# Kernel tuning notes

Hardware: AMD Instinct MI355X
Metric: run time of the kernel (lower is better)

## Reference

```python
import jax, jax.numpy as jnp
import numpy as np

B, S, O = 65536, 32, 16  # batch, state_dim, observation_dim


def setup_inputs() -> dict:
    key = jax.random.key(0)
    k1, k2, k3, k4 = jax.random.split(key, 4)
    observation = jax.random.normal(k1, (B, O), dtype=jnp.float32)
    # SPD observation noise covariance per batch element
    L = 0.1 * jax.random.normal(k2, (B, O, O), dtype=jnp.float32)
    observation_noise = jnp.einsum('bij,bkj->bik', L, L) + 1e-3 * jnp.eye(O, dtype=jnp.float32)
    observation_matrix = 0.001 * jax.random.normal(k3, (O, S), dtype=jnp.float32)
    observation_bias = 1e-6 * jax.random.normal(k4, (O,), dtype=jnp.float32)
    prior_mean = jnp.zeros((S,), dtype=jnp.float32)
    prior_precision = jnp.eye(S, dtype=jnp.float32)
    return {
        'observation': observation,
        'observation_noise': observation_noise,
        'observation_matrix': observation_matrix,
        'observation_bias': observation_bias,
        'prior_mean': prior_mean,
        'prior_precision': prior_precision,
    }


def reference(observation, observation_noise, observation_matrix, observation_bias,
              prior_mean, prior_precision):
    # observation: [B, O]; observation_noise: [B, O, O]
    noise_prec = jnp.linalg.inv(observation_noise)                      # [B, O, O]
    HtR = jnp.einsum('os,bop->bsp', observation_matrix, noise_prec)     # H^T R^{-1}: [B, S, O]
    innovation_cov = jnp.einsum('bso,ot->bst', HtR, observation_matrix) # [B, S, S]
    posterior_covariance = jnp.linalg.inv(prior_precision + innovation_cov)  # [B, S, S]
    residual = jnp.einsum('bso,bo->bs', HtR, observation - observation_bias)[..., None]  # [B, S, 1]
    prior_term = (prior_precision @ prior_mean)[:, None]                # [S, 1]
    posterior_mean = posterior_covariance @ (prior_term + residual)     # [B, S, 1]
    return posterior_mean, posterior_covariance
```

## Files before the change

kernel.cpp:

```cpp
#include <hip/hip_runtime.h>
#include <hip/hip_bf16.h>


typedef __attribute__((ext_vector_type(8))) short bf16x8;
typedef __attribute__((ext_vector_type(4))) float f32x4;

__device__ __forceinline__ unsigned bf16rne(float f) {
    unsigned x = __float_as_uint(f);
    return (x + 0x7FFFu + ((x >> 16) & 1u)) >> 16;
}
__device__ __forceinline__ unsigned pack2(float a, float b) {
    return bf16rne(a) | (bf16rne(b) << 16);
}

__global__ void lgs_setup(const float* __restrict__ H, const float* __restrict__ bias,
                          const float* __restrict__ mu0, const float* __restrict__ P,
                          float* __restrict__ ws)
{
    __shared__ float aug[32][65];
    __shared__ float colk[32];
    __shared__ float Gs[16][32];
    __shared__ float Gts[32][16];
    const int tid = threadIdx.x;

    for (int idx = tid; idx < 2048; idx += 256) {
        int r = idx >> 6, c = idx & 63;
        aug[r][c] = (c < 32) ? P[r * 32 + c] : (((c - 32) == r) ? 1.0f : 0.0f);
    }
    __syncthreads();

    for (int k = 0; k < 32; ++k) {
        if (tid < 32) colk[tid] = aug[tid][k];
        __syncthreads();
        if (tid < 64) {
            float rk = aug[k][tid] * (1.0f / colk[k]);
            aug[k][tid] = rk;
            for (int r = 0; r < 32; ++r)
                if (r != k) aug[r][tid] -= colk[r] * rk;
        }
        __syncthreads();
    }

    for (int idx = tid; idx < 512; idx += 256) {
        int o = idx >> 5, s = idx & 31;
        float acc = 0.f;
        for (int v = 0; v < 32; ++v) acc += H[o * 32 + v] * aug[v][32 + s];
        Gs[o][s] = acc;
    }
    for (int idx = tid; idx < 512; idx += 256) {
        int s = idx >> 4, o = idx & 15;
        float acc = 0.f;
        for (int v = 0; v < 32; ++v) acc += aug[s][32 + v] * H[o * 32 + v];
        Gts[s][o] = acc;
    }
    __syncthreads();

    for (int idx = tid; idx < 256; idx += 256) {
        int j = idx >> 4, i = idx & 15;
        float acc = 0.f;
        for (int s = 0; s < 32; ++s) acc += Gs[i][s] * H[j * 32 + s];
        ws[idx] = acc;
    }
    unsigned* wsu = (unsigned*)ws;
    for (int idx = tid; idx < 512; idx += 256) {
        int r = idx >> 8, rem = idx & 255;
        int l = rem >> 2, j = rem & 3;
        int mm = 16 * r + (l & 15);
        int kb = (((l >> 4) * 8) + 2 * j) & 15;
        wsu[768 + idx] = pack2(-0.5f * Gts[mm][kb], -0.5f * Gts[mm][kb + 1]);
    }
    for (int idx = tid; idx < 1024; idx += 256) {
        int tt = idx >> 8, rem = idx & 255;
        int l = rem >> 2, j = rem & 3;
        int row = 16 * (tt >> 1) + ((l >> 4) << 2) + j;
        int col = 16 * (tt & 1) + (l & 15);
        ws[1280 + idx] = aug[row][32 + col];
    }
    for (int idx = tid; idx < 512; idx += 256) {
        int c = idx >> 8, rem = idx & 255;
        int l = rem >> 2, j2 = rem & 3;
        int col = 16 * c + (l & 15);
        int k = (((l >> 4) * 8) + 2 * j2) & 15;
        wsu[2304 + idx] = pack2(0.5f * Gs[k][col], 0.5f * Gs[k + 1][col]);
    }
    if (tid < 16) {
        float acc = bias[tid];
        for (int s = 0; s < 32; ++s) acc += H[tid * 32 + s] * mu0[s];
        ws[2816 + tid] = acc;
    }
    if (tid < 32) ws[2832 + tid] = mu0[tid];
}

#define BCAST16(x, K) __int_as_float(__builtin_amdgcn_ds_swizzle(__float_as_int(x), (((K) << 5) | 0x10)))

template <int K>
__device__ __forceinline__ void gj16(int t, float (&m)[16], float (&v)[16])
{
    if (t == K) m[K] = 1.0f / m[K];
    float bc[16];
#pragma unroll
    for (int i = 0; i < 16; ++i) bc[i] = BCAST16(m[i], K);
    float pk = m[K] * bc[K];
#pragma unroll
    for (int i = 0; i < 16; ++i)
        if (i != K) m[i] -= bc[i] * pk;
    m[K] = pk;
    float a = v[K] * bc[K];
#pragma unroll
    for (int i = 0; i < 16; ++i)
        if (i != K) v[i] -= bc[i] * a;
    v[K] = a;
}

__global__ __launch_bounds__(512, 4) void lgs_main(
    const float* __restrict__ obs, const float* __restrict__ noise,
    const float* __restrict__ ws,
    float* __restrict__ out_mean, float* __restrict__ out_cov, int B)
{
    __shared__ float ld[8192];

    const int tid  = threadIdx.x;
    const int l    = tid & 63;
    const int t    = tid & 15;
    const int slot = tid >> 4;
    const int wv   = tid >> 6;
    const int b    = blockIdx.x * 32 + slot;
    const int bb   = (b < B) ? b : (B - 1);

    const float* __restrict__ Acm  = ws;
    const float* __restrict__ cvec = ws + 2816;
    const float* __restrict__ m0v  = ws + 2832;

    float m[16], v[16];

    const float4* Rr = (const float4*)(noise + (size_t)bb * 256 + t * 16);
    const float4* Ar = (const float4*)(Acm + t * 16);
#pragma unroll
    for (int i = 0; i < 4; ++i) {
        float4 r = Rr[i], a = Ar[i];
        m[4*i+0] = r.x + a.x; m[4*i+1] = r.y + a.y;
        m[4*i+2] = r.z + a.z; m[4*i+3] = r.w + a.w;
    }
#pragma unroll
    for (int i = 0; i < 16; ++i) v[i] = (i == t) ? 1.0f : 0.0f;

    gj16<0>(t, m, v);   gj16<1>(t, m, v);   gj16<2>(t, m, v);   gj16<3>(t, m, v);
    gj16<4>(t, m, v);   gj16<5>(t, m, v);   gj16<6>(t, m, v);   gj16<7>(t, m, v);
    gj16<8>(t, m, v);   gj16<9>(t, m, v);   gj16<10>(t, m, v);  gj16<11>(t, m, v);
    gj16<12>(t, m, v);  gj16<13>(t, m, v);  gj16<14>(t, m, v);  gj16<15>(t, m, v);

    {
        const int xw = t & 3;
        float* wb = &ld[slot * 256 + t * 16];
        *(float4*)&wb[(0 ^ xw) << 2] = make_float4(v[0],  v[1],  v[2],  v[3]);
        *(float4*)&wb[(1 ^ xw) << 2] = make_float4(v[4],  v[5],  v[6],  v[7]);
        *(float4*)&wb[(2 ^ xw) << 2] = make_float4(v[8],  v[9],  v[10], v[11]);
        *(float4*)&wb[(3 ^ xw) << 2] = make_float4(v[12], v[13], v[14], v[15]);
    }

    const uint4*  AF4 = (const uint4*)(ws + 768);
    const uint4*  BG4 = (const uint4*)(ws + 2304);
    const float4* PF4 = (const float4*)(ws + 1280);
    uint4 a0u = AF4[l], a1u = AF4[64 + l];
    uint4 g0u = BG4[l], g1u = BG4[64 + l];
    bf16x8 A0, A1, Bg0, Bg1;
    __builtin_memcpy(&A0,  &a0u, 16);
    __builtin_memcpy(&A1,  &a1u, 16);
    __builtin_memcpy(&Bg0, &g0u, 16);
    __builtin_memcpy(&Bg1, &g1u, 16);
    float4 pq;
    f32x4 pfr0, pfr1, pfr2, pfr3;
    pq = PF4[l];        pfr0[0]=pq.x; pfr0[1]=pq.y; pfr0[2]=pq.z; pfr0[3]=pq.w;
    pq = PF4[64 + l];   pfr1[0]=pq.x; pfr1[1]=pq.y; pfr1[2]=pq.z; pfr1[3]=pq.w;
    pq = PF4[128 + l];  pfr2[0]=pq.x; pfr2[1]=pq.y; pfr2[2]=pq.z; pfr2[3]=pq.w;
    pq = PF4[192 + l];  pfr3[0]=pq.x; pfr3[1]=pq.y; pfr3[2]=pq.z; pfr3[3]=pq.w;

    const int ch = l & 15;
    const int gp = l >> 4;
    const int gq = (gp & 1) * 2;
    const int xq = ch & 3;
    const int xt = (ch & 1) << 2;
    const float4 cv = ((const float4*)cvec)[gp];
    const float mu0a = m0v[ch], mu0b = m0v[16 + ch];
    const f32x4 zero = {0.f, 0.f, 0.f, 0.f};

#pragma unroll
    for (int h = 0; h < 4; ++h) {
        const int sh  = wv * 4 + h;
        const int bh  = blockIdx.x * 32 + sh;
        const int bhc = (bh < B) ? bh : (B - 1);

        const float* qb = &ld[sh * 256 + ch * 16];
        float4 qa = *(const float4*)&qb[((gq    ) ^ xq) << 2];
        float4 qc = *(const float4*)&qb[((gq + 1) ^ xq) << 2];
        unsigned qarr[4] = { pack2(qa.x, qa.y), pack2(qa.z, qa.w),
                             pack2(qc.x, qc.y), pack2(qc.z, qc.w) };
        bf16x8 Qa; __builtin_memcpy(&Qa, qarr, 16);
        f32x4 d0 = __builtin_amdgcn_mfma_f32_16x16x32_bf16(Qa, Bg0, zero, 0, 0, 0);
        f32x4 d1 = __builtin_amdgcn_mfma_f32_16x16x32_bf16(Qa, Bg1, zero, 0, 0, 0);

        float4 yv = *(const float4*)(obs + (size_t)bhc * 16 + gp * 4);
        float z0 = yv.x - cv.x, z1 = yv.y - cv.y, z2 = yv.z - cv.z, z3 = yv.w - cv.w;
        float p0 = d0[0]*z0 + d0[1]*z1 + d0[2]*z2 + d0[3]*z3;
        float p1 = d1[0]*z0 + d1[1]*z1 + d1[2]*z2 + d1[3]*z3;
        p0 += __int_as_float(__builtin_amdgcn_ds_swizzle(__float_as_int(p0), 0x401F));
        p1 += __int_as_float(__builtin_amdgcn_ds_swizzle(__float_as_int(p1), 0x401F));
        p0 += __shfl_xor(p0, 32, 64);
        p1 += __shfl_xor(p1, 32, 64);
        if (bh < B) {
            if (gp == 0) out_mean[(size_t)bh * 32 + ch]      = mu0a + p0;
            if (gp == 1) out_mean[(size_t)bh * 32 + 16 + ch] = mu0b + p1;
        }

        unsigned* tb = (unsigned*)&ld[sh * 256];
        const int g2 = gp * 2;
        *(uint2*)&tb[      ch * 8 + (g2 ^ xt)] =
            make_uint2(pack2(d0[0], d0[1]), pack2(d0[2], d0[3]));
        *(uint2*)&tb[128 + ch * 8 + (g2 ^ xt)] =
            make_uint2(pack2(d1[0], d1[1]), pack2(d1[2], d1[3]));

        const int kp = (gp & 1) * 4;
        uint4 bu0 = *(const uint4*)&tb[      ch * 8 + (kp ^ xt)];
        uint4 bu1 = *(const uint4*)&tb[128 + ch * 8 + (kp ^ xt)];
        bf16x8 Bf0, Bf1;
        __builtin_memcpy(&Bf0, &bu0, 16);
        __builtin_memcpy(&Bf1, &bu1, 16);
        f32x4 s00 = __builtin_amdgcn_mfma_f32_16x16x32_bf16(A0, Bf0, pfr0, 0, 0, 0);
        f32x4 s01 = __builtin_amdgcn_mfma_f32_16x16x32_bf16(A0, Bf1, pfr1, 0, 0, 0);
        f32x4 s10 = __builtin_amdgcn_mfma_f32_16x16x32_bf16(A1, Bf0, pfr2, 0, 0, 0);
        f32x4 s11 = __builtin_amdgcn_mfma_f32_16x16x32_bf16(A1, Bf1, pfr3, 0, 0, 0);

        if (bh < B) {
            float* Sb = out_cov + (size_t)bh * 1024 + (gp * 4) * 32 + ch;
#pragma unroll
            for (int j = 0; j < 4; ++j) {
                Sb[j * 32]       = s00[j];
                Sb[j * 32 + 16]  = s01[j];
                Sb[j * 32 + 512] = s10[j];
                Sb[j * 32 + 528] = s11[j];
            }
        }
    }
}

extern "C" void kernel_launch(void* const* d_in, const int* in_sizes, int n_in,
                              void* d_out, int out_size, void* d_ws, size_t ws_size,
                              hipStream_t stream)
{
    const float* obs   = (const float*)d_in[0];
    const float* noise = (const float*)d_in[1];
    const float* H     = (const float*)d_in[2];
    const float* bias  = (const float*)d_in[3];
    const float* mu0   = (const float*)d_in[4];
    const float* P     = (const float*)d_in[5];
    float* ws = (float*)d_ws;

    const int B = in_sizes[0] / 16;
    float* out_mean = (float*)d_out;
    float* out_cov  = out_mean + (size_t)B * 32;

    lgs_setup<<<1, 256, 0, stream>>>(H, bias, mu0, P, ws);
    lgs_main<<<(B + 31) / 32, 512, 0, stream>>>(obs, noise, ws, out_mean, out_cov, B);
}
```

Measured before the change: 115.4 us.

## Use in-place negated sweep inversion with 8 lanes per matrix

Replaces the augmented Gauss-Jordan inversion, which used 16 lanes per matrix and a separate identity block, with an in-place sweep operator. Each lane now holds two rows, so a wave inverts 8 matrices and a block covers 64 batch elements. The sweep yields the negated inverse, and the sign is absorbed by flipping the setup constants and the residual. The inverse is also stored to LDS already packed as bf16, which halves LDS use per matrix. The LDS tile is reused for the two d-halves one after the other, with compiler memory barriers to keep the stores and loads in order. This cuts VGPR pressure and the redundant identity-column work, at the cost of more serial work per lane and a longer loop over 8 batches per wave.

```diff
diff --git a/kernel.cpp b/kernel.cpp
--- a/kernel.cpp
+++ b/kernel.cpp
@@ -67,7 +67,7 @@
         int l = rem >> 2, j = rem & 3;
         int mm = 16 * r + (l & 15);
         int kb = (((l >> 4) * 8) + 2 * j) & 15;
-        wsu[768 + idx] = pack2(-0.5f * Gts[mm][kb], -0.5f * Gts[mm][kb + 1]);
+        wsu[768 + idx] = pack2(0.5f * Gts[mm][kb], 0.5f * Gts[mm][kb + 1]);
     }
     for (int idx = tid; idx < 1024; idx += 256) {
         int tt = idx >> 8, rem = idx & 255;
@@ -91,25 +91,32 @@
     if (tid < 32) ws[2832 + tid] = mu0[tid];
 }
 
-#define BCAST16(x, K) __int_as_float(__builtin_amdgcn_ds_swizzle(__float_as_int(x), (((K) << 5) | 0x10)))
+#define BCAST8(x, K) __int_as_float(__builtin_amdgcn_ds_swizzle(__float_as_int(x), (((K) << 5) | 0x18)))
 
 template <int K>
-__device__ __forceinline__ void gj16(int t, float (&m)[16], float (&v)[16])
-{
-    if (t == K) m[K] = 1.0f / m[K];
+__device__ __forceinline__ void sweep_step(int l, float (&m0)[16], float (&m1)[16])
+{
+    const bool own = (l & 7) == (K & 7);
+    float (&mp)[16] = (K >> 3) ? m1 : m0;
+    float (&mo)[16] = (K >> 3) ? m0 : m1;
+    if (own) mp[K] = 1.0f / mp[K];
     float bc[16];
 #pragma unroll
-    for (int i = 0; i < 16; ++i) bc[i] = BCAST16(m[i], K);
-    float pk = m[K] * bc[K];
-#pragma unroll
-    for (int i = 0; i < 16; ++i)
-        if (i != K) m[i] -= bc[i] * pk;
-    m[K] = pk;
-    float a = v[K] * bc[K];
-#pragma unroll
-    for (int i = 0; i < 16; ++i)
-        if (i != K) v[i] -= bc[i] * a;
-    v[K] = a;
+    for (int i = 0; i < 16; ++i) bc[i] = BCAST8(mp[i], K & 7);
+    float fp = own ? 0.0f : mp[K] * bc[K];
+    float fo = mo[K] * bc[K];
+#pragma unroll
+    for (int i = 0; i < 16; ++i) {
+        if (i != K) { mp[i] -= bc[i] * fp; mo[i] -= bc[i] * fo; }
+    }
+    mp[K] = fp;
+    mo[K] = fo;
+    if (own) {
+        float invd = bc[K];
+#pragma unroll
+        for (int i = 0; i < 16; ++i) mp[i] = bc[i] * invd;
+        mp[K] = -invd;
+    }
 }
 
 __global__ __launch_bounds__(512, 4) void lgs_main(
@@ -117,46 +124,58 @@
     const float* __restrict__ ws,
     float* __restrict__ out_mean, float* __restrict__ out_cov, int B)
 {
-    __shared__ float ld[8192];
+    __shared__ unsigned ldu[8192];
 
     const int tid  = threadIdx.x;
     const int l    = tid & 63;
-    const int t    = tid & 15;
-    const int slot = tid >> 4;
     const int wv   = tid >> 6;
-    const int b    = blockIdx.x * 32 + slot;
+    const int g    = l & 7;
+    const int slot = wv * 8 + (l >> 3);
+    const int b    = blockIdx.x * 64 + slot;
     const int bb   = (b < B) ? b : (B - 1);
 
     const float* __restrict__ Acm  = ws;
     const float* __restrict__ cvec = ws + 2816;
     const float* __restrict__ m0v  = ws + 2832;
 
-    float m[16], v[16];
-
-    const float4* Rr = (const float4*)(noise + (size_t)bb * 256 + t * 16);
-    const float4* Ar = (const float4*)(Acm + t * 16);
+    float m0[16], m1[16];
+
+    const float4* Rr0 = (const float4*)(noise + (size_t)bb * 256 + g * 16);
+    const float4* Ar0 = (const float4*)(Acm + g * 16);
+    const float4* Rr1 = (const float4*)(noise + (size_t)bb * 256 + (g + 8) * 16);
+    const float4* Ar1 = (const float4*)(Acm + (g + 8) * 16);
 #pragma unroll
     for (int i = 0; i < 4; ++i) {
-        float4 r = Rr[i], a = Ar[i];
-        m[4*i+0] = r.x + a.x; m[4*i+1] = r.y + a.y;
-        m[4*i+2] = r.z + a.z; m[4*i+3] = r.w + a.w;
-    }
-#pragma unroll
-    for (int i = 0; i < 16; ++i) v[i] = (i == t) ? 1.0f : 0.0f;
-
-    gj16<0>(t, m, v);   gj16<1>(t, m, v);   gj16<2>(t, m, v);   gj16<3>(t, m, v);
-    gj16<4>(t, m, v);   gj16<5>(t, m, v);   gj16<6>(t, m, v);   gj16<7>(t, m, v);
-    gj16<8>(t, m, v);   gj16<9>(t, m, v);   gj16<10>(t, m, v);  gj16<11>(t, m, v);
-    gj16<12>(t, m, v);  gj16<13>(t, m, v);  gj16<14>(t, m, v);  gj16<15>(t, m, v);
+        float4 r = Rr0[i], a = Ar0[i];
+        m0[4*i+0] = r.x + a.x; m0[4*i+1] = r.y + a.y;
+        m0[4*i+2] = r.z + a.z; m0[4*i+3] = r.w + a.w;
+        float4 r1 = Rr1[i], a1 = Ar1[i];
+        m1[4*i+0] = r1.x + a1.x; m1[4*i+1] = r1.y + a1.y;
+        m1[4*i+2] = r1.z + a1.z; m1[4*i+3] = r1.w + a1.w;
+    }
+
+    sweep_step<0>(l, m0, m1);   sweep_step<1>(l, m0, m1);
+    sweep_step<2>(l, m0, m1);   sweep_step<3>(l, m0, m1);
+    sweep_step<4>(l, m0, m1);   sweep_step<5>(l, m0, m1);
+    sweep_step<6>(l, m0, m1);   sweep_step<7>(l, m0, m1);
+    sweep_step<8>(l, m0, m1);   sweep_step<9>(l, m0, m1);
+    sweep_step<10>(l, m0, m1);  sweep_step<11>(l, m0, m1);
+    sweep_step<12>(l, m0, m1);  sweep_step<13>(l, m0, m1);
+    sweep_step<14>(l, m0, m1);  sweep_step<15>(l, m0, m1);
 
     {
-        const int xw = t & 3;
-        float* wb = &ld[slot * 256 + t * 16];
-        *(float4*)&wb[(0 ^ xw) << 2] = make_float4(v[0],  v[1],  v[2],  v[3]);
-        *(float4*)&wb[(1 ^ xw) << 2] = make_float4(v[4],  v[5],  v[6],  v[7]);
-        *(float4*)&wb[(2 ^ xw) << 2] = make_float4(v[8],  v[9],  v[10], v[11]);
-        *(float4*)&wb[(3 ^ xw) << 2] = make_float4(v[12], v[13], v[14], v[15]);
-    }
+        unsigned* qb = &ldu[slot * 128 + g * 8];
+        const int x0 = g & 4;
+        *(uint4*)&qb[x0]      = make_uint4(pack2(m0[0],m0[1]),  pack2(m0[2],m0[3]),
+                                           pack2(m0[4],m0[5]),  pack2(m0[6],m0[7]));
+        *(uint4*)&qb[x0 ^ 4]  = make_uint4(pack2(m0[8],m0[9]),  pack2(m0[10],m0[11]),
+                                           pack2(m0[12],m0[13]), pack2(m0[14],m0[15]));
+        *(uint4*)&qb[64 + x0] = make_uint4(pack2(m1[0],m1[1]),  pack2(m1[2],m1[3]),
+                                           pack2(m1[4],m1[5]),  pack2(m1[6],m1[7]));
+        *(uint4*)&qb[64 + (x0 ^ 4)] = make_uint4(pack2(m1[8],m1[9]),  pack2(m1[10],m1[11]),
+                                                 pack2(m1[12],m1[13]), pack2(m1[14],m1[15]));
+    }
+    asm volatile("" ::: "memory");
 
     const uint4*  AF4 = (const uint4*)(ws + 768);
     const uint4*  BG4 = (const uint4*)(ws + 2304);
@@ -175,32 +194,30 @@
     pq = PF4[128 + l];  pfr2[0]=pq.x; pfr2[1]=pq.y; pfr2[2]=pq.z; pfr2[3]=pq.w;
     pq = PF4[192 + l];  pfr3[0]=pq.x; pfr3[1]=pq.y; pfr3[2]=pq.z; pfr3[3]=pq.w;
 
-    const int ch = l & 15;
-    const int gp = l >> 4;
-    const int gq = (gp & 1) * 2;
-    const int xq = ch & 3;
-    const int xt = (ch & 1) << 2;
+    const int ch   = l & 15;
+    const int gp   = l >> 4;
+    const int qoff = ch * 8 + (((gp & 1) * 4) ^ (ch & 4));
+    const int xt   = (ch & 1) << 2;
+    const int g2   = gp * 2;
+    const int kp   = (gp & 1) * 4;
     const float4 cv = ((const float4*)cvec)[gp];
     const float mu0a = m0v[ch], mu0b = m0v[16 + ch];
     const f32x4 zero = {0.f, 0.f, 0.f, 0.f};
 
 #pragma unroll
-    for (int h = 0; h < 4; ++h) {
-        const int sh  = wv * 4 + h;
-        const int bh  = blockIdx.x * 32 + sh;
+    for (int h = 0; h < 8; ++h) {
+        const int sh  = wv * 8 + h;
+        const int bh  = blockIdx.x * 64 + sh;
         const int bhc = (bh < B) ? bh : (B - 1);
-
-        const float* qb = &ld[sh * 256 + ch * 16];
-        float4 qa = *(const float4*)&qb[((gq    ) ^ xq) << 2];
-        float4 qc = *(const float4*)&qb[((gq + 1) ^ xq) << 2];
-        unsigned qarr[4] = { pack2(qa.x, qa.y), pack2(qa.z, qa.w),
-                             pack2(qc.x, qc.y), pack2(qc.z, qc.w) };
-        bf16x8 Qa; __builtin_memcpy(&Qa, qarr, 16);
+        unsigned* tb = &ldu[sh * 128];
+
+        uint4 qu = *(const uint4*)&tb[qoff];
+        bf16x8 Qa; __builtin_memcpy(&Qa, &qu, 16);
         f32x4 d0 = __builtin_amdgcn_mfma_f32_16x16x32_bf16(Qa, Bg0, zero, 0, 0, 0);
         f32x4 d1 = __builtin_amdgcn_mfma_f32_16x16x32_bf16(Qa, Bg1, zero, 0, 0, 0);
 
         float4 yv = *(const float4*)(obs + (size_t)bhc * 16 + gp * 4);
-        float z0 = yv.x - cv.x, z1 = yv.y - cv.y, z2 = yv.z - cv.z, z3 = yv.w - cv.w;
+        float z0 = cv.x - yv.x, z1 = cv.y - yv.y, z2 = cv.z - yv.z, z3 = cv.w - yv.w;
         float p0 = d0[0]*z0 + d0[1]*z1 + d0[2]*z2 + d0[3]*z3;
         float p1 = d1[0]*z0 + d1[1]*z1 + d1[2]*z2 + d1[3]*z3;
         p0 += __int_as_float(__builtin_amdgcn_ds_swizzle(__float_as_int(p0), 0x401F));
@@ -212,23 +229,24 @@
             if (gp == 1) out_mean[(size_t)bh * 32 + 16 + ch] = mu0b + p1;
         }
 
-        unsigned* tb = (unsigned*)&ld[sh * 256];
-        const int g2 = gp * 2;
-        *(uint2*)&tb[      ch * 8 + (g2 ^ xt)] =
+        asm volatile("" ::: "memory");
+        *(uint2*)&tb[ch * 8 + (g2 ^ xt)] =
             make_uint2(pack2(d0[0], d0[1]), pack2(d0[2], d0[3]));
-        *(uint2*)&tb[128 + ch * 8 + (g2 ^ xt)] =
+        asm volatile("" ::: "memory");
+        uint4 bu0 = *(const uint4*)&tb[ch * 8 + (kp ^ xt)];
+        bf16x8 Bf0; __builtin_memcpy(&Bf0, &bu0, 16);
+        f32x4 s00 = __builtin_amdgcn_mfma_f32_16x16x32_bf16(A0, Bf0, pfr0, 0, 0, 0);
+        f32x4 s10 = __builtin_amdgcn_mfma_f32_16x16x32_bf16(A1, Bf0, pfr2, 0, 0, 0);
+
+        asm volatile("" ::: "memory");
+        *(uint2*)&tb[ch * 8 + (g2 ^ xt)] =
             make_uint2(pack2(d1[0], d1[1]), pack2(d1[2], d1[3]));
-
-        const int kp = (gp & 1) * 4;
-        uint4 bu0 = *(const uint4*)&tb[      ch * 8 + (kp ^ xt)];
-        uint4 bu1 = *(const uint4*)&tb[128 + ch * 8 + (kp ^ xt)];
-        bf16x8 Bf0, Bf1;
-        __builtin_memcpy(&Bf0, &bu0, 16);
-        __builtin_memcpy(&Bf1, &bu1, 16);
-        f32x4 s00 = __builtin_amdgcn_mfma_f32_16x16x32_bf16(A0, Bf0, pfr0, 0, 0, 0);
+        asm volatile("" ::: "memory");
+        uint4 bu1 = *(const uint4*)&tb[ch * 8 + (kp ^ xt)];
+        bf16x8 Bf1; __builtin_memcpy(&Bf1, &bu1, 16);
         f32x4 s01 = __builtin_amdgcn_mfma_f32_16x16x32_bf16(A0, Bf1, pfr1, 0, 0, 0);
-        f32x4 s10 = __builtin_amdgcn_mfma_f32_16x16x32_bf16(A1, Bf0, pfr2, 0, 0, 0);
         f32x4 s11 = __builtin_amdgcn_mfma_f32_16x16x32_bf16(A1, Bf1, pfr3, 0, 0, 0);
+        asm volatile("" ::: "memory");
 
         if (bh < B) {
             float* Sb = out_cov + (size_t)bh * 1024 + (gp * 4) * 32 + ch;
@@ -260,5 +278,5 @@
     float* out_cov  = out_mean + (size_t)B * 32;
 
     lgs_setup<<<1, 256, 0, stream>>>(H, bias, mu0, P, ws);
-    lgs_main<<<(B + 31) / 32, 512, 0, stream>>>(obs, noise, ws, out_mean, out_cov, B);
-}
+    lgs_main<<<(B + 63) / 64, 512, 0, stream>>>(obs, noise, ws, out_mean, out_cov, B);
+}
```

After: 214.2 us. 1.86x slower.
